# Kernel tuning notes

Hardware: AMD Instinct MI355X
Metric: run time of the kernel (lower is better)

## Reference

```python
import jax, jax.numpy as jnp
import numpy as np

N = 5000        # nodes (repo uses 'sample/5000')
D_IN = 512      # feature dim
D_OUT = 16      # output_dim
K = 3           # num meta-paths
N_CLASSES = 100 # num_Labels
P_EDGE = 0.0064 # ~32 avg degree


def setup_inputs() -> dict:
    key = jax.random.key(0)
    ks = jax.random.split(key, 8)
    features = jax.random.normal(ks[0], (N, D_IN), dtype=jnp.float32)
    # sparse binary similarity matrices, symmetrized
    adj = (jax.random.uniform(ks[1], (K, N, N)) < P_EDGE).astype(jnp.float32)
    adj = jnp.maximum(adj, adj.transpose(0, 2, 1))
    W_gnn = jax.random.normal(ks[2], (K, D_IN, D_OUT), dtype=jnp.float32) / np.sqrt(D_IN).astype(np.float32)
    b_gnn = jnp.zeros((K, D_OUT), dtype=jnp.float32)
    att_w = jax.random.normal(ks[3], (K, 2 * D_OUT, 1), dtype=jnp.float32)  # as in torch.randn
    W_final = jax.random.normal(ks[4], (D_OUT, N_CLASSES), dtype=jnp.float32) / np.sqrt(D_OUT).astype(np.float32)
    b_final = jnp.zeros((N_CLASSES,), dtype=jnp.float32)
    return dict(features=features, adj=adj, W_gnn=W_gnn, b_gnn=b_gnn,
                att_w=att_w, W_final=W_final, b_final=b_final)


def _gcn_norm(A_bin):
    # GCNConv normalization: D^{-1/2} (A + I) D^{-1/2} with unit edge weights
    n = A_bin.shape[-1]
    Ahat = A_bin + jnp.eye(n, dtype=A_bin.dtype)
    dinv = jax.lax.rsqrt(Ahat.sum(-1))  # deg >= 1 due to self loops
    return dinv[..., :, None] * Ahat * dinv[..., None, :]


def reference(features, adj, W_gnn, b_gnn, att_w, W_final, b_final):
    # --- per-meta-path GCNConv (edge weights are all 1, from nonzero pattern) ---
    norm = _gcn_norm((adj != 0).astype(features.dtype))          # [K,N,N]
    XW = jnp.einsum('nd,kdo->kno', features, W_gnn)              # [K,N,Dout]
    h = jnp.einsum('knm,kmo->kno', norm, XW) + b_gnn[:, None, :]
    f_meta = jnp.max(h, axis=0)                                  # 'max' aggregation, [N,Dout]

    # --- pairwise attention over meta-paths (vectorized NxN loop) ---
    d = f_meta.shape[1]
    a = f_meta @ att_w[:, :d, 0].T   # [N,K] contribution of f_meta[i]
    b = f_meta @ att_w[:, d:, 0].T   # [N,K] contribution of f_meta[j]
    scores = jnp.exp(jax.nn.relu(a[:, None, :] + b[None, :, :]))  # [N,N,K]
    attn = scores / scores.sum(-1, keepdims=True)

    # --- fuse meta-path adjacencies ---
    A_meta = jnp.einsum('nmk,knm->nm', attn, adj)                # [N,N]

    # --- final GCNConv on the nonzero pattern of A_meta (unit edge weights) ---
    norm_meta = _gcn_norm((A_meta != 0).astype(features.dtype))
    predictions = norm_meta @ (f_meta @ W_final) + b_final
    return f_meta, A_meta, predictions
```

## Files before the change

kernel.cpp:

```cpp
#include <hip/hip_runtime.h>
#include <hip/hip_bf16.h>
#include <cstdint>
#include <cstddef>

#define N_NODES 5000
#define DIN 512
#define DOUT 16
#define KMP 3
#define NCLS 100
#define WSTRIDE 160
#define NWORDS 157
#define NQ 1250
#define CAPK 160
#define CAPU 320

__global__ void k1_bits_deg_nbr(const float* __restrict__ adj,
                                uint32_t* __restrict__ planes,
                                float* __restrict__ dinv,
                                uint16_t* __restrict__ nbrK,
                                int* __restrict__ cntK) {
    int row = blockIdx.x;
    int t   = threadIdx.x;
    int lane = t & 63;
    int wv   = t >> 6;
    const float* arow = adj + (size_t)row * N_NODES;
    __shared__ uint32_t nib32[320];
    __shared__ int wtot[4];
    uint8_t* nib = (uint8_t*)nib32;
    #pragma unroll
    for (int it = 0; it < 5; ++it) {
        int q = it * 256 + t;
        uint32_t m = 0;
        if (q < NQ) {
            float4 v = *(const float4*)(arow + 4 * q);
            m = (v.x != 0.f ? 1u : 0u) | (v.y != 0.f ? 2u : 0u) |
                (v.z != 0.f ? 4u : 0u) | (v.w != 0.f ? 8u : 0u);
        }
        nib[q] = (uint8_t)m;
    }
    __syncthreads();
    uint32_t word = 0;
    int cnt = 0;
    if (t < NWORDS) {
        uint32_t lo = nib32[2 * t], hi = nib32[2 * t + 1];
        word = (lo & 0xFu) | ((lo >> 4) & 0xF0u) | ((lo >> 8) & 0xF00u) | ((lo >> 12) & 0xF000u)
             | ((hi << 16) & 0xF0000u) | ((hi << 12) & 0xF00000u)
             | ((hi << 8) & 0xF000000u) | ((hi << 4) & 0xF0000000u);
        planes[(size_t)row * WSTRIDE + t] = word;
        cnt = __popc(word);
    }
    int x = cnt;
    #pragma unroll
    for (int s = 1; s < 64; s <<= 1) {
        int y = __shfl_up(x, s);
        if (lane >= s) x += y;
    }
    if (lane == 63) wtot[wv] = x;
    __syncthreads();
    int prefix = 0;
    #pragma unroll
    for (int w = 0; w < 4; ++w) if (w < wv) prefix += wtot[w];
    int total = wtot[0] + wtot[1] + wtot[2] + wtot[3];
    int pos = prefix + x - cnt;
    uint16_t* out = nbrK + (size_t)row * CAPK;
    while (word) {
        int b = __builtin_ctz(word);
        word &= word - 1;
        if (pos < CAPK) out[pos] = (uint16_t)(32 * t + b);
        ++pos;
    }
    if (t == 0) {
        dinv[row] = rsqrtf(1.0f + (float)total);
        cntK[row] = (total < CAPK) ? total : CAPK;
    }
}

__global__ void k_union(const uint32_t* __restrict__ planes,
                        uint16_t* __restrict__ nbrU, int* __restrict__ cntU,
                        float* __restrict__ udinv) {
    int i = blockIdx.x;
    int lane = threadIdx.x;
    const uint32_t* p0 = planes + (size_t)i * WSTRIDE;
    const uint32_t* p1 = planes + (size_t)(N_NODES + i) * WSTRIDE;
    const uint32_t* p2 = planes + (size_t)(2 * N_NODES + i) * WSTRIDE;
    uint32_t w0 = p0[lane] | p1[lane] | p2[lane];
    uint32_t w1 = p0[lane + 64] | p1[lane + 64] | p2[lane + 64];
    uint32_t w2 = 0;
    if (lane + 128 < NWORDS) w2 = p0[lane + 128] | p1[lane + 128] | p2[lane + 128];
    int cnt = __popc(w0) + __popc(w1) + __popc(w2);
    int x = cnt;
    #pragma unroll
    for (int s = 1; s < 64; s <<= 1) {
        int y = __shfl_up(x, s);
        if (lane >= s) x += y;
    }
    int pos = x - cnt;
    int total = __shfl(x, 63);
    uint16_t* out = nbrU + (size_t)i * CAPU;
    uint32_t ws[3] = {w0, w1, w2};
    #pragma unroll
    for (int p = 0; p < 3; ++p) {
        uint32_t word = ws[p];
        int base = 32 * (lane + 64 * p);
        while (word) {
            int b = __builtin_ctz(word);
            word &= word - 1;
            if (pos < CAPU) out[pos] = (uint16_t)(base + b);
            ++pos;
        }
    }
    if (lane == 0) {
        cntU[i] = (total < CAPU) ? total : CAPU;
        udinv[i] = rsqrtf(1.0f + (float)total);
    }
}

__global__ void k2a_wt(const float* __restrict__ W, float* __restrict__ Wt) {
    int t = blockIdx.x * blockDim.x + threadIdx.x;
    if (t >= KMP * DIN * DOUT) return;
    int d = t % DIN; int rest = t / DIN; int o = rest % DOUT; int k = rest / DOUT;
    Wt[t] = W[((size_t)k * DIN + d) * DOUT + o];
}

__global__ void k2b_xwd(const float* __restrict__ feat, const float* __restrict__ Wt,
                        const float* __restrict__ dinv, float* __restrict__ XWd) {
    int t = blockIdx.x * blockDim.x + threadIdx.x;
    if (t >= N_NODES * DOUT) return;
    int o = t & 15; int j = t >> 4;
    const float4* f4 = (const float4*)(feat + (size_t)j * DIN);
    const float4* w0 = (const float4*)(Wt + (size_t)(0 * DOUT + o) * DIN);
    const float4* w1 = (const float4*)(Wt + (size_t)(1 * DOUT + o) * DIN);
    const float4* w2 = (const float4*)(Wt + (size_t)(2 * DOUT + o) * DIN);
    float a0 = 0.f, a1 = 0.f, a2 = 0.f;
    #pragma unroll 2
    for (int d4 = 0; d4 < DIN / 4; ++d4) {
        float4 f = f4[d4];
        float4 b0 = w0[d4], b1 = w1[d4], b2 = w2[d4];
        a0 += f.x * b0.x + f.y * b0.y + f.z * b0.z + f.w * b0.w;
        a1 += f.x * b1.x + f.y * b1.y + f.z * b1.z + f.w * b1.w;
        a2 += f.x * b2.x + f.y * b2.y + f.z * b2.z + f.w * b2.w;
    }
    XWd[(size_t)(0 * N_NODES + j) * DOUT + o] = a0 * dinv[0 * N_NODES + j];
    XWd[(size_t)(1 * N_NODES + j) * DOUT + o] = a1 * dinv[1 * N_NODES + j];
    XWd[(size_t)(2 * N_NODES + j) * DOUT + o] = a2 * dinv[2 * N_NODES + j];
}

__global__ void k34_fmeta_ab_gd(const uint16_t* __restrict__ nbrK, const int* __restrict__ cntK,
                                const float* __restrict__ XWd, const float* __restrict__ dinv,
                                const float* __restrict__ bg, const float* __restrict__ aw,
                                const float* __restrict__ Wf, const float* __restrict__ udinv,
                                float* __restrict__ f_meta, float* __restrict__ a4,
                                float* __restrict__ b4, float* __restrict__ Gd) {
    int t = threadIdx.x;
    int o = t & 15;
    int r = t >> 4;
    int i = blockIdx.x * 4 + r;
    __shared__ float fs[4][17];
    float hmax = -1e30f;
    #pragma unroll
    for (int k = 0; k < KMP; ++k) {
        const float* xw = XWd + (size_t)k * N_NODES * DOUT;
        int row = k * N_NODES + i;
        int nn = cntK[row];
        const uint16_t* nb = nbrK + (size_t)row * CAPK;
        float a0 = xw[i * DOUT + o];
        float a1 = 0.f, a2 = 0.f, a3 = 0.f;
        int n = 0;
        for (; n + 4 <= nn; n += 4) {
            ushort4 jj = *(const ushort4*)(nb + n);
            a0 += xw[(int)jj.x * DOUT + o];
            a1 += xw[(int)jj.y * DOUT + o];
            a2 += xw[(int)jj.z * DOUT + o];
            a3 += xw[(int)jj.w * DOUT + o];
        }
        for (; n < nn; ++n) a0 += xw[(int)nb[n] * DOUT + o];
        float h = dinv[row] * ((a0 + a1) + (a2 + a3)) + bg[k * DOUT + o];
        hmax = fmaxf(hmax, h);
    }
    f_meta[i * DOUT + o] = hmax;
    fs[r][o] = hmax;
    float sa0 = hmax * aw[0 * 32 + o], sb0 = hmax * aw[0 * 32 + 16 + o];
    float sa1 = hmax * aw[1 * 32 + o], sb1 = hmax * aw[1 * 32 + 16 + o];
    float sa2 = hmax * aw[2 * 32 + o], sb2 = hmax * aw[2 * 32 + 16 + o];
    #pragma unroll
    for (int s = 1; s < 16; s <<= 1) {
        sa0 += __shfl_xor(sa0, s, 16); sb0 += __shfl_xor(sb0, s, 16);
        sa1 += __shfl_xor(sa1, s, 16); sb1 += __shfl_xor(sb1, s, 16);
        sa2 += __shfl_xor(sa2, s, 16); sb2 += __shfl_xor(sb2, s, 16);
    }
    if (o < 4) {
        float sa = (o == 0) ? sa0 : (o == 1) ? sa1 : (o == 2) ? sa2 : 0.f;
        float sb = (o == 0) ? sb0 : (o == 1) ? sb1 : (o == 2) ? sb2 : 0.f;
        a4[i * 4 + o] = sa;
        b4[i * 4 + o] = sb;
    }
    __syncthreads();
    float f[DOUT];
    #pragma unroll
    for (int q = 0; q < DOUT; ++q) f[q] = fs[r][q];
    float ud = udinv[i];
    for (int c = o; c < NCLS; c += 16) {
        float acc = 0.f;
        #pragma unroll
        for (int q = 0; q < DOUT; ++q) acc += f[q] * Wf[q * NCLS + c];
        Gd[(size_t)i * NCLS + c] = acc * ud;
    }
}

__device__ __forceinline__ float attn_frac(float x0, float x1, float x2,
                                           uint32_t b0, uint32_t b1, uint32_t b2) {
    float e0 = __expf(fmaxf(x0, 0.f));
    float e1 = __expf(fmaxf(x1, 0.f));
    float e2 = __expf(fmaxf(x2, 0.f));
    float num = (b0 ? e0 : 0.f) + (b1 ? e1 : 0.f) + (b2 ? e2 : 0.f);
    return __fdividef(num, e0 + e1 + e2);
}

__global__ void k5_ameta(const uint32_t* __restrict__ planes,
                         const float* __restrict__ a4, const float* __restrict__ b4,
                         float* __restrict__ Am) {
    int i0 = blockIdx.x * 8;
    int t = threadIdx.x;
    __shared__ float a_s[8][3];
    if (t < 24) { int r = t / 3, k = t % 3; a_s[r][k] = a4[(i0 + r) * 4 + k]; }
    __syncthreads();
    for (int c = 0; c < 5; ++c) {
        int j4 = 4 * (t + 256 * c);
        if (j4 >= N_NODES) break;
        int w = j4 >> 5, sh = j4 & 31;
        const float4* bp = (const float4*)(b4 + (size_t)j4 * 4);
        float4 bj0 = bp[0], bj1 = bp[1], bj2 = bp[2], bj3 = bp[3];
        #pragma unroll
        for (int r = 0; r < 8; ++r) {
            int i = i0 + r;
            uint32_t q0 = planes[(size_t)i * WSTRIDE + w] >> sh;
            uint32_t q1 = planes[(size_t)(N_NODES + i) * WSTRIDE + w] >> sh;
            uint32_t q2 = planes[(size_t)(2 * N_NODES + i) * WSTRIDE + w] >> sh;
            uint32_t un = (q0 | q1 | q2) & 0xFu;
            float4 out = make_float4(0.f, 0.f, 0.f, 0.f);
            if (un) {
                float A0 = a_s[r][0], A1 = a_s[r][1], A2 = a_s[r][2];
                if (un & 1u) out.x = attn_frac(A0 + bj0.x, A1 + bj0.y, A2 + bj0.z, q0 & 1u, q1 & 1u, q2 & 1u);
                if (un & 2u) out.y = attn_frac(A0 + bj1.x, A1 + bj1.y, A2 + bj1.z, q0 & 2u, q1 & 2u, q2 & 2u);
                if (un & 4u) out.z = attn_frac(A0 + bj2.x, A1 + bj2.y, A2 + bj2.z, q0 & 4u, q1 & 4u, q2 & 4u);
                if (un & 8u) out.w = attn_frac(A0 + bj3.x, A1 + bj3.y, A2 + bj3.z, q0 & 8u, q1 & 8u, q2 & 8u);
            }
            *(float4*)(Am + (size_t)i * N_NODES + j4) = out;
        }
    }
}

__global__ void k8_pred(const uint16_t* __restrict__ nbrU, const int* __restrict__ cntU,
                        const float* __restrict__ Gd, const float* __restrict__ udinv,
                        const float* __restrict__ bf, float* __restrict__ pred) {
    int i = blockIdx.x;
    int c = threadIdx.x;
    if (c >= NCLS) return;
    int nn = cntU[i];
    const uint16_t* nb = nbrU + (size_t)i * CAPU;
    float a0 = Gd[(size_t)i * NCLS + c];
    float a1 = 0.f, a2 = 0.f, a3 = 0.f;
    int n = 0;
    for (; n + 4 <= nn; n += 4) {
        ushort4 jj = *(const ushort4*)(nb + n);
        a0 += Gd[(size_t)jj.x * NCLS + c];
        a1 += Gd[(size_t)jj.y * NCLS + c];
        a2 += Gd[(size_t)jj.z * NCLS + c];
        a3 += Gd[(size_t)jj.w * NCLS + c];
    }
    for (; n < nn; ++n) a0 += Gd[(size_t)nb[n] * NCLS + c];
    pred[(size_t)i * NCLS + c] = udinv[i] * ((a0 + a1) + (a2 + a3)) + bf[c];
}

extern "C" void kernel_launch(void* const* d_in, const int* in_sizes, int n_in,
                              void* d_out, int out_size, void* d_ws, size_t ws_size,
                              hipStream_t stream) {
    const float* feat = (const float*)d_in[0];
    const float* adj  = (const float*)d_in[1];
    const float* Wg   = (const float*)d_in[2];
    const float* bg   = (const float*)d_in[3];
    const float* aw   = (const float*)d_in[4];
    const float* Wf   = (const float*)d_in[5];
    const float* bf   = (const float*)d_in[6];

    float* f_meta = (float*)d_out;
    float* Am     = f_meta + (size_t)N_NODES * DOUT;
    float* pred   = Am + (size_t)N_NODES * N_NODES;

    char* ws = (char*)d_ws;
    size_t off = 0;
    auto alloc = [&](size_t bytes) {
        void* p = ws + off;
        off = (off + bytes + 255) & ~(size_t)255;
        return p;
    };
    uint32_t* planes = (uint32_t*)alloc((size_t)KMP * N_NODES * WSTRIDE * 4);
    float* dinv  = (float*)alloc((size_t)KMP * N_NODES * 4);
    float* Wt    = (float*)alloc((size_t)KMP * DOUT * DIN * 4);
    float* XWd   = (float*)alloc((size_t)KMP * N_NODES * DOUT * 4);
    float* a4    = (float*)alloc((size_t)N_NODES * 16);
    float* b4    = (float*)alloc((size_t)N_NODES * 16);
    float* udinv = (float*)alloc((size_t)N_NODES * 4);
    float* Gd    = (float*)alloc((size_t)N_NODES * NCLS * 4);
    uint16_t* nbrK = (uint16_t*)alloc((size_t)KMP * N_NODES * CAPK * 2);
    int*      cntK = (int*)alloc((size_t)KMP * N_NODES * 4);
    uint16_t* nbrU = (uint16_t*)alloc((size_t)N_NODES * CAPU * 2);
    int*      cntU = (int*)alloc((size_t)N_NODES * 4);

    hipLaunchKernelGGL(k1_bits_deg_nbr, dim3(KMP * N_NODES), dim3(256), 0, stream,
                       adj, planes, dinv, nbrK, cntK);
    hipLaunchKernelGGL(k_union, dim3(N_NODES), dim3(64), 0, stream,
                       planes, nbrU, cntU, udinv);
    hipLaunchKernelGGL(k2a_wt, dim3((KMP * DIN * DOUT + 255) / 256), dim3(256), 0, stream, Wg, Wt);
    hipLaunchKernelGGL(k2b_xwd, dim3((N_NODES * DOUT + 255) / 256), dim3(256), 0, stream,
                       feat, Wt, dinv, XWd);
    hipLaunchKernelGGL(k34_fmeta_ab_gd, dim3(N_NODES / 4), dim3(64), 0, stream,
                       nbrK, cntK, XWd, dinv, bg, aw, Wf, udinv, f_meta, a4, b4, Gd);
    hipLaunchKernelGGL(k5_ameta, dim3(N_NODES / 8), dim3(256), 0, stream, planes, a4, b4, Am);
    hipLaunchKernelGGL(k8_pred, dim3(N_NODES), dim3(128), 0, stream, nbrU, cntU, Gd, udinv, bf, pred);
}
```

Before: 636.2 us.

## Merge launches: fuse adjacency scan with union and XW matmul, co-launch Ameta and pred

Seven kernels become three. The first processes all three meta-path rows per node in one block and builds the union neighbour list from registers, so the planes are not re-read. Extra blocks in that same launch compute the unscaled XW product straight from the original weight layout, which removes the transpose kernel. The dinv scaling moves into the gather in the f_meta kernel, and the A_meta and prediction kernels share one launch. This cuts launch overhead and lets independent work overlap, at the cost of an extra dinv gather per neighbour and uncoalesced strided weight reads.

```diff
diff --git a/kernel.cpp b/kernel.cpp
--- a/kernel.cpp
+++ b/kernel.cpp
@@ -1,5 +1,4 @@
 #include <hip/hip_runtime.h>
-#include <hip/hip_bf16.h>
 #include <cstdint>
 #include <cstddef>
 
@@ -13,42 +12,108 @@
 #define NQ 1250
 #define CAPK 160
 #define CAPU 320
-
-__global__ void k1_bits_deg_nbr(const float* __restrict__ adj,
-                                uint32_t* __restrict__ planes,
-                                float* __restrict__ dinv,
-                                uint16_t* __restrict__ nbrK,
-                                int* __restrict__ cntK) {
-    int row = blockIdx.x;
-    int t   = threadIdx.x;
+#define NJT 313
+#define NXW (KMP * NJT)
+
+__global__ __launch_bounds__(256)
+void kA(const float* __restrict__ adj, const float* __restrict__ feat,
+        const float* __restrict__ Wg,
+        uint32_t* __restrict__ planes, float* __restrict__ dinv,
+        float* __restrict__ udinv,
+        uint16_t* __restrict__ nbrK, int* __restrict__ cntK,
+        uint16_t* __restrict__ nbrU, int* __restrict__ cntU,
+        float* __restrict__ XW) {
+    int bid = blockIdx.x;
+    int t = threadIdx.x;
+
+    if (bid >= N_NODES) {
+        int b2 = bid - N_NODES;
+        int k = b2 / NJT;
+        int jt = b2 - k * NJT;
+        int j = jt * 16 + (t >> 4);
+        int o = t & 15;
+        if (j < N_NODES) {
+            const float4* f4 = (const float4*)(feat + (size_t)j * DIN);
+            const float* wk = Wg + (size_t)k * DIN * DOUT + o;
+            float acc = 0.f;
+            #pragma unroll 4
+            for (int d4 = 0; d4 < DIN / 4; ++d4) {
+                float4 f = f4[d4];
+                acc += f.x * wk[(4 * d4 + 0) * DOUT]
+                     + f.y * wk[(4 * d4 + 1) * DOUT]
+                     + f.z * wk[(4 * d4 + 2) * DOUT]
+                     + f.w * wk[(4 * d4 + 3) * DOUT];
+            }
+            XW[((size_t)k * N_NODES + j) * DOUT + o] = acc;
+        }
+        return;
+    }
+
+    int i = bid;
     int lane = t & 63;
     int wv   = t >> 6;
-    const float* arow = adj + (size_t)row * N_NODES;
     __shared__ uint32_t nib32[320];
     __shared__ int wtot[4];
     uint8_t* nib = (uint8_t*)nib32;
-    #pragma unroll
-    for (int it = 0; it < 5; ++it) {
-        int q = it * 256 + t;
-        uint32_t m = 0;
-        if (q < NQ) {
-            float4 v = *(const float4*)(arow + 4 * q);
-            m = (v.x != 0.f ? 1u : 0u) | (v.y != 0.f ? 2u : 0u) |
-                (v.z != 0.f ? 4u : 0u) | (v.w != 0.f ? 8u : 0u);
-        }
-        nib[q] = (uint8_t)m;
-    }
+    uint32_t wsav[KMP];
+
+    #pragma unroll
+    for (int k = 0; k < KMP; ++k) {
+        const float* arow = adj + ((size_t)k * N_NODES + i) * N_NODES;
+        __syncthreads();
+        #pragma unroll
+        for (int it = 0; it < 5; ++it) {
+            int q = it * 256 + t;
+            uint32_t m = 0;
+            if (q < NQ) {
+                float4 v = *(const float4*)(arow + 4 * q);
+                m = (v.x != 0.f ? 1u : 0u) | (v.y != 0.f ? 2u : 0u) |
+                    (v.z != 0.f ? 4u : 0u) | (v.w != 0.f ? 8u : 0u);
+            }
+            nib[q] = (uint8_t)m;
+        }
+        __syncthreads();
+        uint32_t word = 0;
+        int cnt = 0;
+        if (t < NWORDS) {
+            uint32_t lo = nib32[2 * t], hi = nib32[2 * t + 1];
+            word = (lo & 0xFu) | ((lo >> 4) & 0xF0u) | ((lo >> 8) & 0xF00u) | ((lo >> 12) & 0xF000u)
+                 | ((hi << 16) & 0xF0000u) | ((hi << 12) & 0xF00000u)
+                 | ((hi << 8) & 0xF000000u) | ((hi << 4) & 0xF0000000u);
+            planes[((size_t)k * N_NODES + i) * WSTRIDE + t] = word;
+            cnt = __popc(word);
+        }
+        wsav[k] = word;
+        int x = cnt;
+        #pragma unroll
+        for (int s = 1; s < 64; s <<= 1) {
+            int y = __shfl_up(x, s);
+            if (lane >= s) x += y;
+        }
+        if (lane == 63) wtot[wv] = x;
+        __syncthreads();
+        int prefix = 0;
+        #pragma unroll
+        for (int w = 0; w < 4; ++w) if (w < wv) prefix += wtot[w];
+        int total = wtot[0] + wtot[1] + wtot[2] + wtot[3];
+        int pos = prefix + x - cnt;
+        uint16_t* out = nbrK + ((size_t)k * N_NODES + i) * CAPK;
+        uint32_t wtmp = word;
+        while (wtmp) {
+            int b = __builtin_ctz(wtmp);
+            wtmp &= wtmp - 1;
+            if (pos < CAPK) out[pos] = (uint16_t)(32 * t + b);
+            ++pos;
+        }
+        if (t == 0) {
+            dinv[k * N_NODES + i] = rsqrtf(1.0f + (float)total);
+            cntK[k * N_NODES + i] = (total < CAPK) ? total : CAPK;
+        }
+    }
+
     __syncthreads();
-    uint32_t word = 0;
-    int cnt = 0;
-    if (t < NWORDS) {
-        uint32_t lo = nib32[2 * t], hi = nib32[2 * t + 1];
-        word = (lo & 0xFu) | ((lo >> 4) & 0xF0u) | ((lo >> 8) & 0xF00u) | ((lo >> 12) & 0xF000u)
-             | ((hi << 16) & 0xF0000u) | ((hi << 12) & 0xF00000u)
-             | ((hi << 8) & 0xF000000u) | ((hi << 4) & 0xF0000000u);
-        planes[(size_t)row * WSTRIDE + t] = word;
-        cnt = __popc(word);
-    }
+    uint32_t uw = wsav[0] | wsav[1] | wsav[2];
+    int cnt = __popc(uw);
     int x = cnt;
     #pragma unroll
     for (int s = 1; s < 64; s <<= 1) {
@@ -62,91 +127,21 @@
     for (int w = 0; w < 4; ++w) if (w < wv) prefix += wtot[w];
     int total = wtot[0] + wtot[1] + wtot[2] + wtot[3];
     int pos = prefix + x - cnt;
-    uint16_t* out = nbrK + (size_t)row * CAPK;
-    while (word) {
-        int b = __builtin_ctz(word);
-        word &= word - 1;
-        if (pos < CAPK) out[pos] = (uint16_t)(32 * t + b);
+    uint16_t* out = nbrU + (size_t)i * CAPU;
+    while (uw) {
+        int b = __builtin_ctz(uw);
+        uw &= uw - 1;
+        if (pos < CAPU) out[pos] = (uint16_t)(32 * t + b);
         ++pos;
     }
     if (t == 0) {
-        dinv[row] = rsqrtf(1.0f + (float)total);
-        cntK[row] = (total < CAPK) ? total : CAPK;
-    }
-}
-
-__global__ void k_union(const uint32_t* __restrict__ planes,
-                        uint16_t* __restrict__ nbrU, int* __restrict__ cntU,
-                        float* __restrict__ udinv) {
-    int i = blockIdx.x;
-    int lane = threadIdx.x;
-    const uint32_t* p0 = planes + (size_t)i * WSTRIDE;
-    const uint32_t* p1 = planes + (size_t)(N_NODES + i) * WSTRIDE;
-    const uint32_t* p2 = planes + (size_t)(2 * N_NODES + i) * WSTRIDE;
-    uint32_t w0 = p0[lane] | p1[lane] | p2[lane];
-    uint32_t w1 = p0[lane + 64] | p1[lane + 64] | p2[lane + 64];
-    uint32_t w2 = 0;
-    if (lane + 128 < NWORDS) w2 = p0[lane + 128] | p1[lane + 128] | p2[lane + 128];
-    int cnt = __popc(w0) + __popc(w1) + __popc(w2);
-    int x = cnt;
-    #pragma unroll
-    for (int s = 1; s < 64; s <<= 1) {
-        int y = __shfl_up(x, s);
-        if (lane >= s) x += y;
-    }
-    int pos = x - cnt;
-    int total = __shfl(x, 63);
-    uint16_t* out = nbrU + (size_t)i * CAPU;
-    uint32_t ws[3] = {w0, w1, w2};
-    #pragma unroll
-    for (int p = 0; p < 3; ++p) {
-        uint32_t word = ws[p];
-        int base = 32 * (lane + 64 * p);
-        while (word) {
-            int b = __builtin_ctz(word);
-            word &= word - 1;
-            if (pos < CAPU) out[pos] = (uint16_t)(base + b);
-            ++pos;
-        }
-    }
-    if (lane == 0) {
         cntU[i] = (total < CAPU) ? total : CAPU;
         udinv[i] = rsqrtf(1.0f + (float)total);
     }
 }
 
-__global__ void k2a_wt(const float* __restrict__ W, float* __restrict__ Wt) {
-    int t = blockIdx.x * blockDim.x + threadIdx.x;
-    if (t >= KMP * DIN * DOUT) return;
-    int d = t % DIN; int rest = t / DIN; int o = rest % DOUT; int k = rest / DOUT;
-    Wt[t] = W[((size_t)k * DIN + d) * DOUT + o];
-}
-
-__global__ void k2b_xwd(const float* __restrict__ feat, const float* __restrict__ Wt,
-                        const float* __restrict__ dinv, float* __restrict__ XWd) {
-    int t = blockIdx.x * blockDim.x + threadIdx.x;
-    if (t >= N_NODES * DOUT) return;
-    int o = t & 15; int j = t >> 4;
-    const float4* f4 = (const float4*)(feat + (size_t)j * DIN);
-    const float4* w0 = (const float4*)(Wt + (size_t)(0 * DOUT + o) * DIN);
-    const float4* w1 = (const float4*)(Wt + (size_t)(1 * DOUT + o) * DIN);
-    const float4* w2 = (const float4*)(Wt + (size_t)(2 * DOUT + o) * DIN);
-    float a0 = 0.f, a1 = 0.f, a2 = 0.f;
-    #pragma unroll 2
-    for (int d4 = 0; d4 < DIN / 4; ++d4) {
-        float4 f = f4[d4];
-        float4 b0 = w0[d4], b1 = w1[d4], b2 = w2[d4];
-        a0 += f.x * b0.x + f.y * b0.y + f.z * b0.z + f.w * b0.w;
-        a1 += f.x * b1.x + f.y * b1.y + f.z * b1.z + f.w * b1.w;
-        a2 += f.x * b2.x + f.y * b2.y + f.z * b2.z + f.w * b2.w;
-    }
-    XWd[(size_t)(0 * N_NODES + j) * DOUT + o] = a0 * dinv[0 * N_NODES + j];
-    XWd[(size_t)(1 * N_NODES + j) * DOUT + o] = a1 * dinv[1 * N_NODES + j];
-    XWd[(size_t)(2 * N_NODES + j) * DOUT + o] = a2 * dinv[2 * N_NODES + j];
-}
-
 __global__ void k34_fmeta_ab_gd(const uint16_t* __restrict__ nbrK, const int* __restrict__ cntK,
-                                const float* __restrict__ XWd, const float* __restrict__ dinv,
+                                const float* __restrict__ XW, const float* __restrict__ dinv,
                                 const float* __restrict__ bg, const float* __restrict__ aw,
                                 const float* __restrict__ Wf, const float* __restrict__ udinv,
                                 float* __restrict__ f_meta, float* __restrict__ a4,
@@ -159,22 +154,24 @@
     float hmax = -1e30f;
     #pragma unroll
     for (int k = 0; k < KMP; ++k) {
-        const float* xw = XWd + (size_t)k * N_NODES * DOUT;
+        const float* xw = XW + (size_t)k * N_NODES * DOUT;
+        const float* dv = dinv + (size_t)k * N_NODES;
         int row = k * N_NODES + i;
         int nn = cntK[row];
         const uint16_t* nb = nbrK + (size_t)row * CAPK;
-        float a0 = xw[i * DOUT + o];
+        float di = dv[i];
+        float a0 = di * xw[i * DOUT + o];
         float a1 = 0.f, a2 = 0.f, a3 = 0.f;
         int n = 0;
         for (; n + 4 <= nn; n += 4) {
             ushort4 jj = *(const ushort4*)(nb + n);
-            a0 += xw[(int)jj.x * DOUT + o];
-            a1 += xw[(int)jj.y * DOUT + o];
-            a2 += xw[(int)jj.z * DOUT + o];
-            a3 += xw[(int)jj.w * DOUT + o];
-        }
-        for (; n < nn; ++n) a0 += xw[(int)nb[n] * DOUT + o];
-        float h = dinv[row] * ((a0 + a1) + (a2 + a3)) + bg[k * DOUT + o];
+            a0 += dv[jj.x] * xw[(int)jj.x * DOUT + o];
+            a1 += dv[jj.y] * xw[(int)jj.y * DOUT + o];
+            a2 += dv[jj.z] * xw[(int)jj.z * DOUT + o];
+            a3 += dv[jj.w] * xw[(int)jj.w * DOUT + o];
+        }
+        for (; n < nn; ++n) a0 += dv[nb[n]] * xw[(int)nb[n] * DOUT + o];
+        float h = di * ((a0 + a1) + (a2 + a3)) + bg[k * DOUT + o];
         hmax = fmaxf(hmax, h);
     }
     f_meta[i * DOUT + o] = hmax;
@@ -216,60 +213,67 @@
     return __fdividef(num, e0 + e1 + e2);
 }
 
-__global__ void k5_ameta(const uint32_t* __restrict__ planes,
-                         const float* __restrict__ a4, const float* __restrict__ b4,
-                         float* __restrict__ Am) {
-    int i0 = blockIdx.x * 8;
+#define NB_K5 625
+
+__global__ __launch_bounds__(256)
+void kC(const uint32_t* __restrict__ planes,
+        const float* __restrict__ a4, const float* __restrict__ b4,
+        float* __restrict__ Am,
+        const uint16_t* __restrict__ nbrU, const int* __restrict__ cntU,
+        const float* __restrict__ Gd, const float* __restrict__ udinv,
+        const float* __restrict__ bf, float* __restrict__ pred) {
+    int bid = blockIdx.x;
     int t = threadIdx.x;
-    __shared__ float a_s[8][3];
-    if (t < 24) { int r = t / 3, k = t % 3; a_s[r][k] = a4[(i0 + r) * 4 + k]; }
-    __syncthreads();
-    for (int c = 0; c < 5; ++c) {
-        int j4 = 4 * (t + 256 * c);
-        if (j4 >= N_NODES) break;
-        int w = j4 >> 5, sh = j4 & 31;
-        const float4* bp = (const float4*)(b4 + (size_t)j4 * 4);
-        float4 bj0 = bp[0], bj1 = bp[1], bj2 = bp[2], bj3 = bp[3];
-        #pragma unroll
-        for (int r = 0; r < 8; ++r) {
-            int i = i0 + r;
-            uint32_t q0 = planes[(size_t)i * WSTRIDE + w] >> sh;
-            uint32_t q1 = planes[(size_t)(N_NODES + i) * WSTRIDE + w] >> sh;
-            uint32_t q2 = planes[(size_t)(2 * N_NODES + i) * WSTRIDE + w] >> sh;
-            uint32_t un = (q0 | q1 | q2) & 0xFu;
-            float4 out = make_float4(0.f, 0.f, 0.f, 0.f);
-            if (un) {
-                float A0 = a_s[r][0], A1 = a_s[r][1], A2 = a_s[r][2];
-                if (un & 1u) out.x = attn_frac(A0 + bj0.x, A1 + bj0.y, A2 + bj0.z, q0 & 1u, q1 & 1u, q2 & 1u);
-                if (un & 2u) out.y = attn_frac(A0 + bj1.x, A1 + bj1.y, A2 + bj1.z, q0 & 2u, q1 & 2u, q2 & 2u);
-                if (un & 4u) out.z = attn_frac(A0 + bj2.x, A1 + bj2.y, A2 + bj2.z, q0 & 4u, q1 & 4u, q2 & 4u);
-                if (un & 8u) out.w = attn_frac(A0 + bj3.x, A1 + bj3.y, A2 + bj3.z, q0 & 8u, q1 & 8u, q2 & 8u);
+
+    if (bid < NB_K5) {
+        int i0 = bid * 8;
+        __shared__ float a_s[8][3];
+        if (t < 24) { int r = t / 3, k = t % 3; a_s[r][k] = a4[(i0 + r) * 4 + k]; }
+        __syncthreads();
+        for (int c = 0; c < 5; ++c) {
+            int j4 = 4 * (t + 256 * c);
+            if (j4 >= N_NODES) break;
+            int w = j4 >> 5, sh = j4 & 31;
+            const float4* bp = (const float4*)(b4 + (size_t)j4 * 4);
+            float4 bj0 = bp[0], bj1 = bp[1], bj2 = bp[2], bj3 = bp[3];
+            #pragma unroll
+            for (int r = 0; r < 8; ++r) {
+                int i = i0 + r;
+                uint32_t q0 = planes[(size_t)i * WSTRIDE + w] >> sh;
+                uint32_t q1 = planes[(size_t)(N_NODES + i) * WSTRIDE + w] >> sh;
+                uint32_t q2 = planes[(size_t)(2 * N_NODES + i) * WSTRIDE + w] >> sh;
+                uint32_t un = (q0 | q1 | q2) & 0xFu;
+                float4 outv = make_float4(0.f, 0.f, 0.f, 0.f);
+                if (un) {
+                    float A0 = a_s[r][0], A1 = a_s[r][1], A2 = a_s[r][2];
+                    if (un & 1u) outv.x = attn_frac(A0 + bj0.x, A1 + bj0.y, A2 + bj0.z, q0 & 1u, q1 & 1u, q2 & 1u);
+                    if (un & 2u) outv.y = attn_frac(A0 + bj1.x, A1 + bj1.y, A2 + bj1.z, q0 & 2u, q1 & 2u, q2 & 2u);
+                    if (un & 4u) outv.z = attn_frac(A0 + bj2.x, A1 + bj2.y, A2 + bj2.z, q0 & 4u, q1 & 4u, q2 & 4u);
+                    if (un & 8u) outv.w = attn_frac(A0 + bj3.x, A1 + bj3.y, A2 + bj3.z, q0 & 8u, q1 & 8u, q2 & 8u);
+                }
+                *(float4*)(Am + (size_t)i * N_NODES + j4) = outv;
             }
-            *(float4*)(Am + (size_t)i * N_NODES + j4) = out;
-        }
-    }
-}
-
-__global__ void k8_pred(const uint16_t* __restrict__ nbrU, const int* __restrict__ cntU,
-                        const float* __restrict__ Gd, const float* __restrict__ udinv,
-                        const float* __restrict__ bf, float* __restrict__ pred) {
-    int i = blockIdx.x;
-    int c = threadIdx.x;
-    if (c >= NCLS) return;
-    int nn = cntU[i];
-    const uint16_t* nb = nbrU + (size_t)i * CAPU;
-    float a0 = Gd[(size_t)i * NCLS + c];
-    float a1 = 0.f, a2 = 0.f, a3 = 0.f;
-    int n = 0;
-    for (; n + 4 <= nn; n += 4) {
-        ushort4 jj = *(const ushort4*)(nb + n);
-        a0 += Gd[(size_t)jj.x * NCLS + c];
-        a1 += Gd[(size_t)jj.y * NCLS + c];
-        a2 += Gd[(size_t)jj.z * NCLS + c];
-        a3 += Gd[(size_t)jj.w * NCLS + c];
-    }
-    for (; n < nn; ++n) a0 += Gd[(size_t)nb[n] * NCLS + c];
-    pred[(size_t)i * NCLS + c] = udinv[i] * ((a0 + a1) + (a2 + a3)) + bf[c];
+        }
+    } else {
+        int b2 = bid - NB_K5;
+        int i = b2 * 2 + (t >> 7);
+        int c = t & 127;
+        if (c >= NCLS) return;
+        int nn = cntU[i];
+        const uint16_t* nb = nbrU + (size_t)i * CAPU;
+        float a0 = Gd[(size_t)i * NCLS + c];
+        float a1 = 0.f, a2 = 0.f, a3 = 0.f;
+        int n = 0;
+        for (; n + 4 <= nn; n += 4) {
+            ushort4 jj = *(const ushort4*)(nb + n);
+            a0 += Gd[(size_t)jj.x * NCLS + c];
+            a1 += Gd[(size_t)jj.y * NCLS + c];
+            a2 += Gd[(size_t)jj.z * NCLS + c];
+            a3 += Gd[(size_t)jj.w * NCLS + c];
+        }
+        for (; n < nn; ++n) a0 += Gd[(size_t)nb[n] * NCLS + c];
+        pred[(size_t)i * NCLS + c] = udinv[i] * ((a0 + a1) + (a2 + a3)) + bf[c];
+    }
 }
 
 extern "C" void kernel_launch(void* const* d_in, const int* in_sizes, int n_in,
@@ -296,8 +300,7 @@
     };
     uint32_t* planes = (uint32_t*)alloc((size_t)KMP * N_NODES * WSTRIDE * 4);
     float* dinv  = (float*)alloc((size_t)KMP * N_NODES * 4);
-    float* Wt    = (float*)alloc((size_t)KMP * DOUT * DIN * 4);
-    float* XWd   = (float*)alloc((size_t)KMP * N_NODES * DOUT * 4);
+    float* XW    = (float*)alloc((size_t)KMP * N_NODES * DOUT * 4);
     float* a4    = (float*)alloc((size_t)N_NODES * 16);
     float* b4    = (float*)alloc((size_t)N_NODES * 16);
     float* udinv = (float*)alloc((size_t)N_NODES * 4);
@@ -307,15 +310,10 @@
     uint16_t* nbrU = (uint16_t*)alloc((size_t)N_NODES * CAPU * 2);
     int*      cntU = (int*)alloc((size_t)N_NODES * 4);
 
-    hipLaunchKernelGGL(k1_bits_deg_nbr, dim3(KMP * N_NODES), dim3(256), 0, stream,
-                       adj, planes, dinv, nbrK, cntK);
-    hipLaunchKernelGGL(k_union, dim3(N_NODES), dim3(64), 0, stream,
-                       planes, nbrU, cntU, udinv);
-    hipLaunchKernelGGL(k2a_wt, dim3((KMP * DIN * DOUT + 255) / 256), dim3(256), 0, stream, Wg, Wt);
-    hipLaunchKernelGGL(k2b_xwd, dim3((N_NODES * DOUT + 255) / 256), dim3(256), 0, stream,
-                       feat, Wt, dinv, XWd);
+    hipLaunchKernelGGL(kA, dim3(N_NODES + NXW), dim3(256), 0, stream,
+                       adj, feat, Wg, planes, dinv, udinv, nbrK, cntK, nbrU, cntU, XW);
     hipLaunchKernelGGL(k34_fmeta_ab_gd, dim3(N_NODES / 4), dim3(64), 0, stream,
-                       nbrK, cntK, XWd, dinv, bg, aw, Wf, udinv, f_meta, a4, b4, Gd);
-    hipLaunchKernelGGL(k5_ameta, dim3(N_NODES / 8), dim3(256), 0, stream, planes, a4, b4, Am);
-    hipLaunchKernelGGL(k8_pred, dim3(N_NODES), dim3(128), 0, stream, nbrU, cntU, Gd, udinv, bf, pred);
-}
+                       nbrK, cntK, XW, dinv, bg, aw, Wf, udinv, f_meta, a4, b4, Gd);
+    hipLaunchKernelGGL(kC, dim3(NB_K5 + N_NODES / 2), dim3(256), 0, stream,
+                       planes, a4, b4, Am, nbrU, cntU, Gd, udinv, bf, pred);
+}
```

New measurement: 570.3 us. 1.12x faster.
